# Kernel tuning notes

Measured on AMD Instinct MI355X. Metric: run time of the kernel, lower is better.

Reference implementation:

```python
import jax, jax.numpy as jnp
import numpy as np

B, T, F, H, FUT = 64, 512, 64, 512, 96  # batch, past len, features, hidden, future len


def setup_inputs() -> dict:
    key = jax.random.key(0)
    ks = jax.random.split(key, 19)
    s = 1.0 / np.sqrt(H)  # PyTorch LSTM/Linear init scale
    u = lambda k, shape: jax.random.uniform(k, shape, jnp.float32, -s, s)
    inp = {"input_seq": jax.random.normal(ks[0], (B, T, F), jnp.float32)}
    i = 1
    for pre in ("enc", "dec"):
        for l in range(2):
            ins = F if l == 0 else H
            inp[f"{pre}_Wih{l}"] = u(ks[i], (4 * H, ins)); i += 1
            inp[f"{pre}_Whh{l}"] = u(ks[i], (4 * H, H)); i += 1
            inp[f"{pre}_bih{l}"] = u(ks[i], (4 * H,)); i += 1
            inp[f"{pre}_bhh{l}"] = u(ks[i], (4 * H,)); i += 1
    inp["fc_W"] = u(ks[17], (F, H))
    inp["fc_b"] = u(ks[18], (F,))
    return inp


def _cell(x, h, c, Wih, Whh, bih, bhh):
    # PyTorch gate order: i, f, g, o
    g = x @ Wih.T + h @ Whh.T + bih + bhh
    i_, f_, g_, o_ = jnp.split(g, 4, axis=-1)
    c = jax.nn.sigmoid(f_) * c + jax.nn.sigmoid(i_) * jnp.tanh(g_)
    h = jax.nn.sigmoid(o_) * jnp.tanh(c)
    return h, c


def reference(input_seq, enc_Wih0, enc_Whh0, enc_bih0, enc_bhh0,
              enc_Wih1, enc_Whh1, enc_bih1, enc_bhh1,
              dec_Wih0, dec_Whh0, dec_bih0, dec_bhh0,
              dec_Wih1, dec_Whh1, dec_bih1, dec_bhh1,
              fc_W, fc_b):
    b = input_seq.shape[0]
    z = jnp.zeros((b, H), input_seq.dtype)

    def run_layer(x, Wih, Whh, bih, bhh):
        def step(carry, xt):
            h, c = _cell(xt, carry[0], carry[1], Wih, Whh, bih, bhh)
            return (h, c), h
        (h, c), ys = jax.lax.scan(step, (z, z), jnp.swapaxes(x, 0, 1))
        return jnp.swapaxes(ys, 0, 1), h, c

    # encoder (2 layers, eval mode -> no dropout)
    y0, h0, c0 = run_layer(input_seq, enc_Wih0, enc_Whh0, enc_bih0, enc_bhh0)
    _, h1, c1 = run_layer(y0, enc_Wih1, enc_Whh1, enc_bih1, enc_bhh1)

    def dec_step(carry, _):
        x, dh0, dc0, dh1, dc1 = carry
        dh0, dc0 = _cell(x, dh0, dc0, dec_Wih0, dec_Whh0, dec_bih0, dec_bhh0)
        dh1, dc1 = _cell(dh0, dh1, dc1, dec_Wih1, dec_Whh1, dec_bih1, dec_bhh1)
        out = dh1 @ fc_W.T + fc_b
        return (out, dh0, dc0, dh1, dc1), out

    dec_in = input_seq[:, -1, :]
    _, outs = jax.lax.scan(dec_step, (dec_in, h0, c0, h1, c1), None, length=FUT)
    return jnp.swapaxes(outs, 0, 1)  # [B, FUT, F]
```

## Files before the change

### kernel.cpp

```cpp
#include <hip/hip_runtime.h>
#include <stdint.h>

typedef __attribute__((ext_vector_type(8))) short short8;
typedef __attribute__((ext_vector_type(4))) float floatx4;
typedef unsigned short u16;
typedef unsigned int u32;

constexpr int BSZ = 64;
constexpr int SEQT = 512;
constexpr int FIN = 64;
constexpr int HID = 512;
constexpr int NG = 2048;
constexpr int FUTL = 96;
constexpr int K0 = FIN + HID;
constexpr int K1 = HID + HID;
constexpr int K0P = K0 + 8;
constexpr int NGRP = 256;
constexpr int NFCB = 4;
constexpr int NBLK = NGRP + NFCB;
constexpr int NTHR = 256;

constexpr int SLOT_HP = 128 * 256;
constexpr int SLOT_XP = 16 * 256;
constexpr int NSLOT_H = 65;

constexpr size_t S_W0 = (size_t)NG * K0 * 2;
constexpr size_t S_W1 = (size_t)NG * K1 * 2;
constexpr size_t S_FC = (size_t)FIN * HID * 2;

constexpr size_t OFF_WHI_E0 = 0;
constexpr size_t OFF_WLO_E0 = OFF_WHI_E0 + S_W0;
constexpr size_t OFF_WHI_E1 = OFF_WLO_E0 + S_W0;
constexpr size_t OFF_WLO_E1 = OFF_WHI_E1 + S_W1;
constexpr size_t OFF_WHI_D1 = OFF_WLO_E1 + S_W1;
constexpr size_t OFF_WLO_D1 = OFF_WHI_D1 + S_W1;
constexpr size_t OFF_WFH   = OFF_WLO_D1 + S_W1;
constexpr size_t OFF_WFL   = OFF_WFH + S_W1;
constexpr size_t OFF_FCHI  = OFF_WFL + S_W1;
constexpr size_t OFF_FCLO  = OFF_FCHI + S_FC;
constexpr size_t OFF_GX    = OFF_FCLO + S_FC;
constexpr size_t OFF_BEFF  = OFF_GX + (size_t)NG * BSZ * 4;
constexpr size_t OFF_XP    = OFF_BEFF + (size_t)NG * 4;
constexpr size_t OFF_H0P   = OFF_XP + (size_t)SEQT * SLOT_XP * 4;
constexpr size_t OFF_H1P   = OFF_H0P + (size_t)NSLOT_H * SLOT_HP * 4;
constexpr size_t OFF_CNT   = OFF_H1P + (size_t)NSLOT_H * SLOT_HP * 4;
constexpr size_t CNT_BYTES = 65536;

#define FCF(c)   ((c) + 0)
#define DONE0(c) ((c) + 256)
#define DONE1(c) ((c) + 2304)
#define GOA0(c)  ((c) + 4352)
#define GOB0(c)  ((c) + 6400)
#define GOA1(c)  ((c) + 8448)
#define GOB1(c)  ((c) + 10496)

__device__ __forceinline__ u16 f2bf(float f) {
  u32 u = __float_as_uint(f);
  u += 0x7FFFu + ((u >> 16) & 1u);
  return (u16)(u >> 16);
}
__device__ __forceinline__ float bf2f(u16 h) { return __uint_as_float(((u32)h) << 16); }
__device__ __forceinline__ u32 packsplit(float v) {
  u16 h = f2bf(v);
  u16 l = f2bf(v - bf2f(h));
  return (u32)h | ((u32)l << 16);
}

__device__ __forceinline__ float sigf(float x) { return 1.f / (1.f + __expf(-x)); }
__device__ __forceinline__ float tanh_f(float x) {
  float xx = fminf(20.f, fmaxf(-20.f, x));
  float e = __expf(-2.f * xx);
  return (1.f - e) / (1.f + e);
}

__device__ __forceinline__ floatx4 mfma3(short8 ah, short8 al, short8 bh, short8 bl, floatx4 acc) {
  acc = __builtin_amdgcn_mfma_f32_16x16x32_bf16(ah, bh, acc, 0, 0, 0);
  acc = __builtin_amdgcn_mfma_f32_16x16x32_bf16(ah, bl, acc, 0, 0, 0);
  acc = __builtin_amdgcn_mfma_f32_16x16x32_bf16(al, bh, acc, 0, 0, 0);
  return acc;
}

__device__ __forceinline__ void st_sc_u32(u32* p, u32 v) {
  asm volatile("global_store_dword %0, %1, off sc0 sc1" :: "v"(p), "v"(v) : "memory");
}
#define WAITVM0() asm volatile("s_waitcnt vmcnt(0)" ::: "memory")

#define ALD(p) __hip_atomic_load((p), __ATOMIC_RELAXED, __HIP_MEMORY_SCOPE_AGENT)
#define AST(p, v) __hip_atomic_store((p), (v), __ATOMIC_RELAXED, __HIP_MEMORY_SCOPE_AGENT)

__device__ __forceinline__ int slotof(int u) { return u < 0 ? 0 : ((u & 63) + 1); }

__device__ __forceinline__ void ld_frag(const u32* p, short8& ah, short8& al) {
  uint4 a = *(const uint4*)p;
  uint4 b = *(const uint4*)(p + 256);
  union { u32 u[4]; short8 s; } H, L;
  H.u[0] = __builtin_amdgcn_perm(a.y, a.x, 0x05040100u);
  L.u[0] = __builtin_amdgcn_perm(a.y, a.x, 0x07060302u);
  H.u[1] = __builtin_amdgcn_perm(a.w, a.z, 0x05040100u);
  L.u[1] = __builtin_amdgcn_perm(a.w, a.z, 0x07060302u);
  H.u[2] = __builtin_amdgcn_perm(b.y, b.x, 0x05040100u);
  L.u[2] = __builtin_amdgcn_perm(b.y, b.x, 0x07060302u);
  H.u[3] = __builtin_amdgcn_perm(b.w, b.z, 0x05040100u);
  L.u[3] = __builtin_amdgcn_perm(b.w, b.z, 0x07060302u);
  ah = H.s; al = L.s;
}

__global__ void k_split_pair(const float* __restrict__ Wih, const float* __restrict__ Whh,
                             int ins, int K, u16* __restrict__ hi, u16* __restrict__ lo) {
  int n = NG * K;
  for (int idx = blockIdx.x * blockDim.x + threadIdx.x; idx < n; idx += gridDim.x * blockDim.x) {
    int row = idx / K;
    int k = idx - row * K;
    float v = (k < ins) ? Wih[row * ins + k] : Whh[row * HID + (k - ins)];
    u16 h = f2bf(v);
    hi[idx] = h;
    lo[idx] = f2bf(v - bf2f(h));
  }
}

__global__ void k_split_flat(const float* __restrict__ src, u16* __restrict__ hi,
                             u16* __restrict__ lo, int n) {
  for (int idx = blockIdx.x * blockDim.x + threadIdx.x; idx < n; idx += gridDim.x * blockDim.x) {
    float v = src[idx];
    u16 h = f2bf(v);
    hi[idx] = h;
    lo[idx] = f2bf(v - bf2f(h));
  }
}

__global__ void k_fuse(const float* __restrict__ dWih0, const float* __restrict__ dWhh0,
                       const float* __restrict__ fcW,
                       u16* __restrict__ wfh, u16* __restrict__ wfl) {
  __shared__ float wr[FIN];
  const int row = blockIdx.x;
  if (threadIdx.x < FIN) wr[threadIdx.x] = dWih0[row * FIN + threadIdx.x];
  __syncthreads();
  for (int j = threadIdx.x; j < HID; j += blockDim.x) {
    float acc = 0.f;
#pragma unroll
    for (int f = 0; f < FIN; ++f) acc = fmaf(wr[f], fcW[f * HID + j], acc);
    u16 h = f2bf(acc);
    wfh[(size_t)row * K1 + j] = h;
    wfl[(size_t)row * K1 + j] = f2bf(acc - bf2f(h));
    float v2 = dWhh0[row * HID + j];
    u16 h2 = f2bf(v2);
    wfh[(size_t)row * K1 + HID + j] = h2;
    wfl[(size_t)row * K1 + HID + j] = f2bf(v2 - bf2f(h2));
  }
}

__global__ void k_gx(const float* __restrict__ dWih0, const float* __restrict__ in_seq,
                     const float* __restrict__ fcb, const float* __restrict__ bdih0,
                     const float* __restrict__ bdhh0, float* __restrict__ gx,
                     float* __restrict__ beff) {
  __shared__ float xl[BSZ * FIN];
  __shared__ float fb[FIN];
  const int row0 = blockIdx.x * 8;
  for (int i = threadIdx.x; i < BSZ * FIN; i += blockDim.x) {
    int b = i >> 6, f = i & 63;
    xl[i] = in_seq[(b * SEQT + (SEQT - 1)) * FIN + f];
  }
  if (threadIdx.x < FIN) fb[threadIdx.x] = fcb[threadIdx.x];
  __syncthreads();
  for (int i = threadIdx.x; i < 8 * BSZ; i += blockDim.x) {
    int r = row0 + (i >> 6);
    int b = i & 63;
    float acc = 0.f;
#pragma unroll 8
    for (int f = 0; f < FIN; ++f)
      acc = fmaf(dWih0[r * FIN + f], xl[(b << 6) + f] - fb[f], acc);
    gx[r * BSZ + b] = acc;
    if (b == 0) {
      float accb = 0.f;
#pragma unroll 8
      for (int f = 0; f < FIN; ++f) accb = fmaf(dWih0[r * FIN + f], fb[f], accb);
      beff[r] = bdih0[r] + bdhh0[r] + accb;
    }
  }
}

__global__ void k_pack_x(const float* __restrict__ x, u32* __restrict__ xp) {
  int n = BSZ * SEQT * FIN;
  for (int idx = blockIdx.x * blockDim.x + threadIdx.x; idx < n; idx += gridDim.x * blockDim.x) {
    int t = idx / (BSZ * FIN);
    int rem = idx - t * (BSZ * FIN);
    int b = rem >> 6;
    int f = rem & 63;
    u32 pk = packsplit(x[(b * SEQT + t) * FIN + f]);
    int off = ((f >> 2) * 64 + b) * 4 + (f & 3);
    xp[t * SLOT_XP + off] = pk;
  }
}

struct Params {
  const u16 *we0h, *we0l, *we1h, *we1l;
  const u16 *wd1h, *wd1l, *wfh, *wfl;
  const u16 *fch, *fcl;
  const u32 *xp;
  u32 *h0p, *h1p;
  const float *beih0, *behh0, *beih1, *behh1;
  const float *bdih1, *bdhh1;
  const float *gx, *beff;
  const float *fcb;
  float *out;
  u32 *cnt;
};

__device__ void master_wait(u32* own, u32 ownT, u32* fcf, u32 fcT) {
  if (threadIdx.x < 64) {
    int l = threadIdx.x;
    for (;;) {
      bool ok = ALD(own + l * 16) >= ownT && ALD(own + (l + 64) * 16) >= ownT;
      if (fcf && l < 4) ok = ok && ALD(fcf + l * 16) >= fcT;
      if (__all(ok)) break;
      __builtin_amdgcn_s_sleep(1);
    }
  }
  __syncthreads();
}

__device__ void sweep128(u32* arr, u32 T) {
  if (threadIdx.x < 64) {
    int l = threadIdx.x;
    while (!__all(ALD(arr + l * 16) >= T && ALD(arr + (l + 64) * 16) >= T))
      __builtin_amdgcn_s_sleep(1);
  }
  __syncthreads();
}

__device__ __forceinline__ void worker_wait(u32* cell, u32 tok) {
  if (threadIdx.x == 0) {
    while (ALD(cell) < tok) __builtin_amdgcn_s_sleep(1);
  }
  __syncthreads();
}

__device__ __forceinline__ void fence_acq() {
  __builtin_amdgcn_fence(__ATOMIC_ACQUIRE, "agent");
}

__device__ __forceinline__ void arrive(u32* cell, u32 tok) {
  WAITVM0();
  __syncthreads();
  if (threadIdx.x == 0) AST(cell, tok);
}

__device__ __forceinline__ void bcast(u32* goA, u32 tokA, u32* goBF, u32 prog) {
  const int tid = threadIdx.x;
  if (tid >= 1 && tid < 128) AST(goA + (tid << 4), tokA);
  else if (tid >= 128) AST(goBF + ((tid - 128) << 4), prog);
}

template <bool IS_L1>
__device__ void load_w_lds(const u16* __restrict__ gh, const u16* __restrict__ gl,
                           u16* wh, u16* wl, int hc) {
  constexpr int K = IS_L1 ? K1 : K0;
  for (int i = threadIdx.x; i < 16 * K; i += NTHR) {
    int rr, k;
    if (IS_L1) { rr = i >> 10; k = i & 1023; }
    else       { rr = i / K0;  k = i - rr * K0; }
    int gc = ((rr >> 2) * HID) + hc + (rr & 3);
    int dst = IS_L1 ? ((rr << 10) + ((((k >> 3) ^ rr)) << 3) + (k & 7))
                    : (rr * K0P + k);
    wh[dst] = gh[(size_t)gc * K + k];
    wl[dst] = gl[(size_t)gc * K + k];
  }
  __syncthreads();
}

template <bool IS_L1, int KBASE, int LEN>
__device__ __forceinline__ void kpart(const u32* __restrict__ sp,
                                      const u16* __restrict__ wh, const u16* __restrict__ wl,
                                      int r, int quad, int mo, floatx4& acc) {
  const int qo = quad << 3;
  constexpr int NIT = LEN / 32;
  uint4 ra[NIT], rb[NIT];
#pragma unroll
  for (int i = 0; i < NIT; ++i) {
    const u32* p = sp + (((i * 32 + qo) >> 2) << 8) + mo;
    ra[i] = *(const uint4*)p;
    rb[i] = *(const uint4*)(p + 256);
  }
#pragma unroll
  for (int i = 0; i < NIT; ++i) {
    union { u32 u[4]; short8 s; } H, L;
    H.u[0] = __builtin_amdgcn_perm(ra[i].y, ra[i].x, 0x05040100u);
    L.u[0] = __builtin_amdgcn_perm(ra[i].y, ra[i].x, 0x07060302u);
    H.u[1] = __builtin_amdgcn_perm(ra[i].w, ra[i].z, 0x05040100u);
    L.u[1] = __builtin_amdgcn_perm(ra[i].w, ra[i].z, 0x07060302u);
    H.u[2] = __builtin_amdgcn_perm(rb[i].y, rb[i].x, 0x05040100u);
    L.u[2] = __builtin_amdgcn_perm(rb[i].y, rb[i].x, 0x07060302u);
    H.u[3] = __builtin_amdgcn_perm(rb[i].w, rb[i].z, 0x05040100u);
    L.u[3] = __builtin_amdgcn_perm(rb[i].w, rb[i].z, 0x07060302u);
    const int kg = i * 32 + KBASE;
    int woff;
    if (IS_L1) { int c = (kg >> 3) + quad; woff = (r << 10) + ((c ^ r) << 3); }
    else       { woff = r * K0P + kg + qo; }
    short8 bh = *(const short8*)(wh + woff);
    short8 bl = *(const short8*)(wl + woff);
    acc = mfma3(H.s, L.s, bh, bl, acc);
  }
}

__device__ __forceinline__ void epilogue(floatx4 acc, floatx4 bs, float& creg,
                                         u32* __restrict__ oslab,
                                         const float* __restrict__ gxb) {
  const int tid = threadIdx.x, lane = tid & 63;
  const int j = lane & 3;
  const int isel = (lane >> 2) & 3;
  const int slb = lane & 48;
  float gate[4];
#pragma unroll
  for (int q = 0; q < 4; ++q) {
    const int sl = slb + (q << 2) + j;
    float t0 = __shfl(acc[0], sl, 64);
    float t1 = __shfl(acc[1], sl, 64);
    float t2 = __shfl(acc[2], sl, 64);
    float t3 = __shfl(acc[3], sl, 64);
    gate[q] = (isel == 0) ? t0 : (isel == 1) ? t1 : (isel == 2) ? t2 : t3;
  }
  if (gxb != nullptr) {
    const int bb = tid >> 2;
#pragma unroll
    for (int q = 0; q < 4; ++q) gate[q] += gxb[q * (HID * BSZ) + j * BSZ + bb];
  }
  float iv = gate[0] + bs[0];
  float fv = gate[1] + bs[1];
  float gv = gate[2] + bs[2];
  float ov = gate[3] + bs[3];
  float cn = fmaf(sigf(fv), creg, sigf(iv) * tanh_f(gv));
  float hn = sigf(ov) * tanh_f(cn);
  creg = cn;
  st_sc_u32(oslab + tid, packsplit(hn));
}

__device__ void fc_step(int t, int blkq, const u32* __restrict__ h1slot,
                        const u16* __restrict__ fh, const u16* __restrict__ fl,
                        const float* __restrict__ fcb, float* __restrict__ out) {
  const int tid = threadIdx.x, lane = tid & 63, w = tid >> 6;
  const int quad = lane >> 4, r = lane & 15;
  const int m = (w << 4) + r;
  const int qo = quad << 3;
  const int mo = m << 2;
  const int col = (blkq << 4) + r;
  floatx4 acc = {0.f, 0.f, 0.f, 0.f};
#pragma unroll
  for (int kk = 0; kk < HID; kk += 32) {
    short8 ah, al;
    ld_frag(h1slot + (((kk + qo) >> 2) << 8) + mo, ah, al);
    short8 b1 = *(const short8*)(fh + col * HID + kk + qo);
    short8 b2 = *(const short8*)(fl + col * HID + kk + qo);
    acc = mfma3(ah, al, b1, b2, acc);
  }
  float bias = fcb[col];
#pragma unroll
  for (int i = 0; i < 4; ++i) {
    int b = (w << 4) + (quad << 2) + i;
    out[(b * FUTL + t) * FIN + col] = acc[i] + bias;
  }
}

__global__ __launch_bounds__(NTHR, 1) void lstm_coop(Params p) {
  __shared__ u16 wsmem[32768];
  u16* wh = wsmem;
  u16* wl = wsmem + 16 * 1024;
  const int blk = blockIdx.x;
  const int tid = threadIdx.x;

  u32* fcf = FCF(p.cnt);
  u32* d0 = DONE0(p.cnt);
  u32* d1 = DONE1(p.cnt);

  if (blk >= NGRP) {
    const int fi = blk - NGRP;
    for (int t = 0; t < FUTL; ++t) {
      sweep128(d1, (u32)(513 + t));
      if ((t & 63) == 0) fence_acq();
      fc_step(t, fi, p.h1p + (size_t)slotof(512 + t) * SLOT_HP,
              p.fch, p.fcl, p.fcb, p.out);
      WAITVM0();
      __syncthreads();
      if (tid == 0) AST(fcf + fi * 16, (u32)(t + 1));
    }
    return;
  }

  const int grp = blk >> 7;
  const int lidx = blk & 127;
  const int hc = lidx << 2;
  const int lane = tid & 63, w = tid >> 6;
  const int quad = lane >> 4, r = lane & 15;
  const int mo = ((w << 4) + r) << 2;

  u32* goA  = grp ? GOA1(p.cnt) : GOA0(p.cnt);
  u32* goBF = grp ? GOB0(p.cnt) : GOB1(p.cnt);
  u32* myGoA = goA + lidx * 16;
  u32* myGoB = (grp ? GOB1(p.cnt) : GOB0(p.cnt)) + lidx * 16;
  u32* myDone = (grp ? d1 : d0) + lidx * 16;

  floatx4 bse, bsd;
  {
    int ch = hc + (tid & 3);
    const float* bi  = grp ? p.beih1 : p.beih0;
    const float* bh2 = grp ? p.behh1 : p.behh0;
#pragma unroll
    for (int q = 0; q < 4; ++q) {
      bse[q] = bi[q * HID + ch] + bh2[q * HID + ch];
      bsd[q] = grp ? (p.bdih1[q * HID + ch] + p.bdhh1[q * HID + ch])
                   : p.beff[q * HID + ch];
    }
  }
  float creg = 0.f;

  if (!grp) {
    load_w_lds<false>(p.we0h, p.we0l, wh, wl, hc);
    for (int s = 0; s < SEQT; ++s) {
      u32 tok = (u32)(s + 1);
      floatx4 acc = {0.f, 0.f, 0.f, 0.f};
      if (lidx == 0) {
        master_wait(d0, (u32)s, nullptr, 0u);
        if (s >= 63) worker_wait(myGoB, (u32)(s - 63));
        bcast(goA, tok, goBF, (u32)s);
        if ((s & 63) == 0 && s) fence_acq();
        kpart<false, 0, FIN>(p.xp + (size_t)s * SLOT_XP, wh, wl, r, quad, mo, acc);
      } else {
        kpart<false, 0, FIN>(p.xp + (size_t)s * SLOT_XP, wh, wl, r, quad, mo, acc);
        worker_wait(myGoA, tok);
        if ((s & 63) == 0 && s) fence_acq();
      }
      kpart<false, FIN, HID>(p.h0p + (size_t)slotof(s - 1) * SLOT_HP, wh, wl, r, quad, mo, acc);
      epilogue(acc, bse, creg,
               p.h0p + (size_t)slotof(s) * SLOT_HP + (lidx << 8), nullptr);
      arrive(myDone, tok);
    }
    if (lidx == 0) {
      sweep128(d0, 512u);
      if (tid >= 128) AST(goBF + ((tid - 128) << 4), 512u);
    }
    load_w_lds<true>(p.wfh, p.wfl, wh, wl, hc);
    for (int t = 0; t < FUTL; ++t) {
      u32 tok = (u32)(513 + t);
      floatx4 acc = {0.f, 0.f, 0.f, 0.f};
      if (lidx == 0) {
        master_wait(d0, (u32)(512 + t), nullptr, 0u);
        if (t == 0) worker_wait(myGoB, 449u);
        bcast(goA, tok, goBF, (u32)(512 + t));
      } else {
        worker_wait(myGoA, tok);
      }
      if ((t & 63) == 0) fence_acq();
      kpart<true, 512, HID>(p.h0p + (size_t)slotof(511 + t) * SLOT_HP, wh, wl, r, quad, mo, acc);
      if (t) {
        worker_wait(myGoB, (u32)(512 + t));
        kpart<true, 0, HID>(p.h1p + (size_t)slotof(511 + t) * SLOT_HP, wh, wl, r, quad, mo, acc);
      }
      epilogue(acc, bsd, creg,
               p.h0p + (size_t)slotof(512 + t) * SLOT_HP + (lidx << 8),
               (t == 0) ? (p.gx + hc * BSZ) : nullptr);
      arrive(myDone, tok);
    }
    if (lidx == 0) {
      sweep128(d0, 608u);
      if (tid >= 128) AST(goBF + ((tid - 128) << 4), 608u);
    }
  } else {
    load_w_lds<true>(p.we1h, p.we1l, wh, wl, hc);
    for (int t = 0; t < SEQT; ++t) {
      u32 tok = (u32)(t + 1);
      floatx4 acc = {0.f, 0.f, 0.f, 0.f};
      if (lidx == 0) {
        master_wait(d1, (u32)t, nullptr, 0u);
        bcast(goA, tok, goBF, (u32)t);
      } else {
        worker_wait(myGoA, tok);
      }
      if ((t & 63) == 0 && t) fence_acq();
      kpart<true, 512, HID>(p.h1p + (size_t)slotof(t - 1) * SLOT_HP, wh, wl, r, quad, mo, acc);
      worker_wait(myGoB, (u32)(t + 1));
      kpart<true, 0, HID>(p.h0p + (size_t)slotof(t) * SLOT_HP, wh, wl, r, quad, mo, acc);
      epilogue(acc, bse, creg,
               p.h1p + (size_t)slotof(t) * SLOT_HP + (lidx << 8), nullptr);
      arrive(myDone, tok);
    }
    load_w_lds<true>(p.wd1h, p.wd1l, wh, wl, hc);
    for (int t = 0; t < FUTL; ++t) {
      u32 tok = (u32)(513 + t);
      floatx4 acc = {0.f, 0.f, 0.f, 0.f};
      if (lidx == 0) {
        master_wait(d1, (u32)(512 + t), (t >= 64) ? fcf : nullptr, (u32)(t - 63));
        bcast(goA, tok, goBF, (u32)(512 + t));
      } else {
        worker_wait(myGoA, tok);
      }
      if ((t & 63) == 0) fence_acq();
      kpart<true, 512, HID>(p.h1p + (size_t)slotof(511 + t) * SLOT_HP, wh, wl, r, quad, mo, acc);
      worker_wait(myGoB, (u32)(513 + t));
      kpart<true, 0, HID>(p.h0p + (size_t)slotof(512 + t) * SLOT_HP, wh, wl, r, quad, mo, acc);
      epilogue(acc, bsd, creg,
               p.h1p + (size_t)slotof(512 + t) * SLOT_HP + (lidx << 8), nullptr);
      arrive(myDone, tok);
    }
  }
}

extern "C" void kernel_launch(void* const* d_in, const int* in_sizes, int n_in,
                              void* d_out, int out_size, void* d_ws, size_t ws_size,
                              hipStream_t stream) {
  (void)in_sizes; (void)n_in; (void)out_size; (void)ws_size;
  const float* in_seq = (const float*)d_in[0];
  const float* eWih0 = (const float*)d_in[1];
  const float* eWhh0 = (const float*)d_in[2];
  const float* ebih0 = (const float*)d_in[3];
  const float* ebhh0 = (const float*)d_in[4];
  const float* eWih1 = (const float*)d_in[5];
  const float* eWhh1 = (const float*)d_in[6];
  const float* ebih1 = (const float*)d_in[7];
  const float* ebhh1 = (const float*)d_in[8];
  const float* dWih0 = (const float*)d_in[9];
  const float* dWhh0 = (const float*)d_in[10];
  const float* dbih0 = (const float*)d_in[11];
  const float* dbhh0 = (const float*)d_in[12];
  const float* dWih1 = (const float*)d_in[13];
  const float* dWhh1 = (const float*)d_in[14];
  const float* dbih1 = (const float*)d_in[15];
  const float* dbhh1 = (const float*)d_in[16];
  const float* fcW  = (const float*)d_in[17];
  const float* fcb  = (const float*)d_in[18];

  char* ws = (char*)d_ws;
  u16* we0h = (u16*)(ws + OFF_WHI_E0); u16* we0l = (u16*)(ws + OFF_WLO_E0);
  u16* we1h = (u16*)(ws + OFF_WHI_E1); u16* we1l = (u16*)(ws + OFF_WLO_E1);
  u16* wd1h = (u16*)(ws + OFF_WHI_D1); u16* wd1l = (u16*)(ws + OFF_WLO_D1);
  u16* wfh  = (u16*)(ws + OFF_WFH);    u16* wfl  = (u16*)(ws + OFF_WFL);
  u16* fch  = (u16*)(ws + OFF_FCHI);   u16* fcl  = (u16*)(ws + OFF_FCLO);
  float* gx   = (float*)(ws + OFF_GX);
  float* beff = (float*)(ws + OFF_BEFF);
  u32* xp   = (u32*)(ws + OFF_XP);
  u32* h0p  = (u32*)(ws + OFF_H0P);
  u32* h1p  = (u32*)(ws + OFF_H1P);
  u32* cnt  = (u32*)(ws + OFF_CNT);

  hipMemsetAsync(ws + OFF_H0P, 0, (size_t)SLOT_HP * 4, stream);
  hipMemsetAsync(ws + OFF_H1P, 0, (size_t)SLOT_HP * 4, stream);
  hipMemsetAsync(ws + OFF_CNT, 0, CNT_BYTES, stream);

  k_split_pair<<<512, 256, 0, stream>>>(eWih0, eWhh0, FIN, K0, we0h, we0l);
  k_split_pair<<<512, 256, 0, stream>>>(eWih1, eWhh1, HID, K1, we1h, we1l);
  k_split_pair<<<512, 256, 0, stream>>>(dWih1, dWhh1, HID, K1, wd1h, wd1l);
  k_split_flat<<<128, 256, 0, stream>>>(fcW, fch, fcl, FIN * HID);
  k_fuse<<<NG, 256, 0, stream>>>(dWih0, dWhh0, fcW, wfh, wfl);
  k_gx<<<256, 256, 0, stream>>>(dWih0, in_seq, fcb, dbih0, dbhh0, gx, beff);
  k_pack_x<<<1024, 256, 0, stream>>>(in_seq, xp);

  Params p;
  p.we0h = we0h; p.we0l = we0l; p.we1h = we1h; p.we1l = we1l;
  p.wd1h = wd1h; p.wd1l = wd1l; p.wfh = wfh; p.wfl = wfl;
  p.fch = fch; p.fcl = fcl;
  p.xp = xp; p.h0p = h0p; p.h1p = h1p;
  p.beih0 = ebih0; p.behh0 = ebhh0; p.beih1 = ebih1; p.behh1 = ebhh1;
  p.bdih1 = dbih1; p.bdhh1 = dbhh1;
  p.gx = gx; p.beff = beff;
  p.fcb = fcb;
  p.out = (float*)d_out;
  p.cnt = cnt;

  lstm_coop<<<dim3(NBLK), dim3(NTHR), 0, stream>>>(p);
}
```

Measured before the change: 4.272 ms.

## Reorder layer-1 encoder waits, cache progress tokens, drop spin sleeps

Removes s_sleep from the spin-wait loops so waiters react to flag changes sooner. Adds cached-token variants of the waits so a block skips re-polling a counter it has already seen past the target. In the layer-1 encoder loop, non-master blocks now do the input (h0) half of the matvec before waiting on their own layer's go signal, overlapping that work with the layer-1 barrier. The fc-progress check is split out of master_wait into a single-thread wait. Busy spinning without sleep may add memory traffic and contention on the flag cache lines.

```diff
diff --git a/kernel.cpp b/kernel.cpp
--- a/kernel.cpp
+++ b/kernel.cpp
@@ -206,15 +206,10 @@
   u32 *cnt;
 };
 
-__device__ void master_wait(u32* own, u32 ownT, u32* fcf, u32 fcT) {
+__device__ void master_wait(u32* own, u32 ownT) {
   if (threadIdx.x < 64) {
     int l = threadIdx.x;
-    for (;;) {
-      bool ok = ALD(own + l * 16) >= ownT && ALD(own + (l + 64) * 16) >= ownT;
-      if (fcf && l < 4) ok = ok && ALD(fcf + l * 16) >= fcT;
-      if (__all(ok)) break;
-      __builtin_amdgcn_s_sleep(1);
-    }
+    while (!__all(ALD(own + l * 16) >= ownT && ALD(own + (l + 64) * 16) >= ownT)) {}
   }
   __syncthreads();
 }
@@ -230,7 +225,29 @@
 
 __device__ __forceinline__ void worker_wait(u32* cell, u32 tok) {
   if (threadIdx.x == 0) {
-    while (ALD(cell) < tok) __builtin_amdgcn_s_sleep(1);
+    while (ALD(cell) < tok) {}
+  }
+  __syncthreads();
+}
+
+__device__ __forceinline__ void worker_wait_c(u32* cell, u32 tok, u32& cache) {
+  if (threadIdx.x == 0 && cache < tok) {
+    u32 v;
+    do { v = ALD(cell); } while (v < tok);
+    cache = v;
+  }
+  __syncthreads();
+}
+
+__device__ __forceinline__ void fcf_wait_c(u32* fcf, u32 tok, u32& cache) {
+  if (threadIdx.x == 0 && cache < tok) {
+    u32 m;
+    do {
+      u32 a = ALD(fcf), b = ALD(fcf + 16), c = ALD(fcf + 32), d = ALD(fcf + 48);
+      u32 m1 = a < b ? a : b, m2 = c < d ? c : d;
+      m = m1 < m2 ? m1 : m2;
+    } while (m < tok);
+    cache = m;
   }
   __syncthreads();
 }
@@ -413,13 +430,14 @@
   float creg = 0.f;
 
   if (!grp) {
+    u32 d1seen = 0;
     load_w_lds<false>(p.we0h, p.we0l, wh, wl, hc);
     for (int s = 0; s < SEQT; ++s) {
       u32 tok = (u32)(s + 1);
       floatx4 acc = {0.f, 0.f, 0.f, 0.f};
       if (lidx == 0) {
-        master_wait(d0, (u32)s, nullptr, 0u);
-        if (s >= 63) worker_wait(myGoB, (u32)(s - 63));
+        master_wait(d0, (u32)s);
+        if (s >= 63) worker_wait_c(myGoB, (u32)(s - 63), d1seen);
         bcast(goA, tok, goBF, (u32)s);
         if ((s & 63) == 0 && s) fence_acq();
         kpart<false, 0, FIN>(p.xp + (size_t)s * SLOT_XP, wh, wl, r, quad, mo, acc);
@@ -442,8 +460,8 @@
       u32 tok = (u32)(513 + t);
       floatx4 acc = {0.f, 0.f, 0.f, 0.f};
       if (lidx == 0) {
-        master_wait(d0, (u32)(512 + t), nullptr, 0u);
-        if (t == 0) worker_wait(myGoB, 449u);
+        master_wait(d0, (u32)(512 + t));
+        if (t == 0) worker_wait_c(myGoB, 449u, d1seen);
         bcast(goA, tok, goBF, (u32)(512 + t));
       } else {
         worker_wait(myGoA, tok);
@@ -451,7 +469,7 @@
       if ((t & 63) == 0) fence_acq();
       kpart<true, 512, HID>(p.h0p + (size_t)slotof(511 + t) * SLOT_HP, wh, wl, r, quad, mo, acc);
       if (t) {
-        worker_wait(myGoB, (u32)(512 + t));
+        worker_wait_c(myGoB, (u32)(512 + t), d1seen);
         kpart<true, 0, HID>(p.h1p + (size_t)slotof(511 + t) * SLOT_HP, wh, wl, r, quad, mo, acc);
       }
       epilogue(acc, bsd, creg,
@@ -464,20 +482,26 @@
       if (tid >= 128) AST(goBF + ((tid - 128) << 4), 608u);
     }
   } else {
+    u32 d0seen = 0;
+    u32 fcseen = 0;
     load_w_lds<true>(p.we1h, p.we1l, wh, wl, hc);
     for (int t = 0; t < SEQT; ++t) {
       u32 tok = (u32)(t + 1);
       floatx4 acc = {0.f, 0.f, 0.f, 0.f};
       if (lidx == 0) {
-        master_wait(d1, (u32)t, nullptr, 0u);
+        master_wait(d1, (u32)t);
         bcast(goA, tok, goBF, (u32)t);
+        worker_wait_c(myGoB, (u32)(t + 1), d0seen);
+        if ((t & 63) == 0 && t) fence_acq();
+        kpart<true, 0, HID>(p.h0p + (size_t)slotof(t) * SLOT_HP, wh, wl, r, quad, mo, acc);
+        kpart<true, 512, HID>(p.h1p + (size_t)slotof(t - 1) * SLOT_HP, wh, wl, r, quad, mo, acc);
       } else {
+        worker_wait_c(myGoB, (u32)(t + 1), d0seen);
+        if ((t & 63) == 0 && t) fence_acq();
+        kpart<true, 0, HID>(p.h0p + (size_t)slotof(t) * SLOT_HP, wh, wl, r, quad, mo, acc);
         worker_wait(myGoA, tok);
+        kpart<true, 512, HID>(p.h1p + (size_t)slotof(t - 1) * SLOT_HP, wh, wl, r, quad, mo, acc);
       }
-      if ((t & 63) == 0 && t) fence_acq();
-      kpart<true, 512, HID>(p.h1p + (size_t)slotof(t - 1) * SLOT_HP, wh, wl, r, quad, mo, acc);
-      worker_wait(myGoB, (u32)(t + 1));
-      kpart<true, 0, HID>(p.h0p + (size_t)slotof(t) * SLOT_HP, wh, wl, r, quad, mo, acc);
       epilogue(acc, bse, creg,
                p.h1p + (size_t)slotof(t) * SLOT_HP + (lidx << 8), nullptr);
       arrive(myDone, tok);
@@ -487,14 +511,15 @@
       u32 tok = (u32)(513 + t);
       floatx4 acc = {0.f, 0.f, 0.f, 0.f};
       if (lidx == 0) {
-        master_wait(d1, (u32)(512 + t), (t >= 64) ? fcf : nullptr, (u32)(t - 63));
+        master_wait(d1, (u32)(512 + t));
+        if (t >= 64) fcf_wait_c(fcf, (u32)(t - 63), fcseen);
         bcast(goA, tok, goBF, (u32)(512 + t));
       } else {
         worker_wait(myGoA, tok);
       }
       if ((t & 63) == 0) fence_acq();
       kpart<true, 512, HID>(p.h1p + (size_t)slotof(511 + t) * SLOT_HP, wh, wl, r, quad, mo, acc);
-      worker_wait(myGoB, (u32)(513 + t));
+      worker_wait_c(myGoB, (u32)(513 + t), d0seen);
       kpart<true, 0, HID>(p.h0p + (size_t)slotof(512 + t) * SLOT_HP, wh, wl, r, quad, mo, acc);
       epilogue(acc, bsd, creg,
                p.h1p + (size_t)slotof(512 + t) * SLOT_HP + (lidx << 8), nullptr);
```

Result: faster. 3.529 ms (median of 2 runs) (-17.4%).

## Restructure inter-block synchronization with packed progress counters and dedicated masters

Applied to the files above, without the earlier changes.

Replaces the per-block padded done flags and the two-level go-flag broadcast with packed progress arrays (one u32 per block, contiguous). Dedicated master loops run on spare FC blocks for the encoder phases. Other waits sweep the packed arrays directly, cache the observed minimum so repeated sweeps can be skipped, and drop the s_sleep backoff. The layer-1 encoder also reorders its two partial matmuls so the h0 input term is computed before waiting on its own recurrence. The aim is to cut per-step barrier latency on the serial recurrence. The cost is more polling traffic on adjacent words, and the change risks contention or ordering bugs in the reworked protocol.

```diff
diff --git a/kernel.cpp b/kernel.cpp
--- a/kernel.cpp
+++ b/kernel.cpp
@@ -47,12 +47,10 @@
 constexpr size_t CNT_BYTES = 65536;
 
 #define FCF(c)   ((c) + 0)
-#define DONE0(c) ((c) + 256)
-#define DONE1(c) ((c) + 2304)
-#define GOA0(c)  ((c) + 4352)
-#define GOB0(c)  ((c) + 6400)
-#define GOA1(c)  ((c) + 8448)
-#define GOB1(c)  ((c) + 10496)
+#define PK0(c)   ((c) + 256)
+#define PK1(c)   ((c) + 384)
+#define GOA0(c)  ((c) + 512)
+#define GOA1(c)  ((c) + 2560)
 
 __device__ __forceinline__ u16 f2bf(float f) {
   u32 u = __float_as_uint(f);
@@ -206,23 +204,27 @@
   u32 *cnt;
 };
 
-__device__ void master_wait(u32* own, u32 ownT, u32* fcf, u32 fcT) {
+__device__ __forceinline__ void sweep_pk_c(const u32* pk, u32 target, u32& cache) {
+  if (threadIdx.x < 64 && cache < target) {
+    u32 a, b;
+    do {
+      a = ALD(pk + threadIdx.x);
+      b = ALD(pk + threadIdx.x + 64);
+    } while (!__all(a >= target && b >= target));
+    u32 m = a < b ? a : b;
+#pragma unroll
+    for (int off = 1; off < 64; off <<= 1) {
+      u32 o = __shfl_xor(m, off, 64);
+      m = o < m ? o : m;
+    }
+    cache = m;
+  }
+  __syncthreads();
+}
+
+__device__ void sweep_pk_sleep(const u32* pk, u32 target) {
   if (threadIdx.x < 64) {
-    int l = threadIdx.x;
-    for (;;) {
-      bool ok = ALD(own + l * 16) >= ownT && ALD(own + (l + 64) * 16) >= ownT;
-      if (fcf && l < 4) ok = ok && ALD(fcf + l * 16) >= fcT;
-      if (__all(ok)) break;
-      __builtin_amdgcn_s_sleep(1);
-    }
-  }
-  __syncthreads();
-}
-
-__device__ void sweep128(u32* arr, u32 T) {
-  if (threadIdx.x < 64) {
-    int l = threadIdx.x;
-    while (!__all(ALD(arr + l * 16) >= T && ALD(arr + (l + 64) * 16) >= T))
+    while (!__all(ALD(pk + threadIdx.x) >= target && ALD(pk + threadIdx.x + 64) >= target))
       __builtin_amdgcn_s_sleep(1);
   }
   __syncthreads();
@@ -230,7 +232,20 @@
 
 __device__ __forceinline__ void worker_wait(u32* cell, u32 tok) {
   if (threadIdx.x == 0) {
-    while (ALD(cell) < tok) __builtin_amdgcn_s_sleep(1);
+    while (ALD(cell) < tok) {}
+  }
+  __syncthreads();
+}
+
+__device__ __forceinline__ void fcf_wait_c(u32* fcf, u32 tok, u32& cache) {
+  if (threadIdx.x == 0 && cache < tok) {
+    u32 m;
+    do {
+      u32 a = ALD(fcf), b = ALD(fcf + 16), c = ALD(fcf + 32), d = ALD(fcf + 48);
+      u32 m1 = a < b ? a : b, m2 = c < d ? c : d;
+      m = m1 < m2 ? m1 : m2;
+    } while (m < tok);
+    cache = m;
   }
   __syncthreads();
 }
@@ -245,10 +260,23 @@
   if (threadIdx.x == 0) AST(cell, tok);
 }
 
-__device__ __forceinline__ void bcast(u32* goA, u32 tokA, u32* goBF, u32 prog) {
-  const int tid = threadIdx.x;
-  if (tid >= 1 && tid < 128) AST(goA + (tid << 4), tokA);
-  else if (tid >= 128) AST(goBF + ((tid - 128) << 4), prog);
+__device__ void enc_master(const u32* pkOwn, const u32* pkFore, u32* goA, bool farlag) {
+  for (int s = 0; s < SEQT; ++s) {
+    if (threadIdx.x < 64) {
+      int l = threadIdx.x;
+      for (;;) {
+        bool ok = ALD(pkOwn + l) >= (u32)s && ALD(pkOwn + l + 64) >= (u32)s;
+        if (farlag && s >= 63) {
+          u32 ft = (u32)(s - 63);
+          ok = ok && ALD(pkFore + l) >= ft && ALD(pkFore + l + 64) >= ft;
+        }
+        if (__all(ok)) break;
+      }
+    }
+    __syncthreads();
+    if (threadIdx.x < 128) AST(goA + (threadIdx.x << 4), (u32)(s + 1));
+    __syncthreads();
+  }
 }
 
 template <bool IS_L1>
@@ -368,13 +396,15 @@
   const int tid = threadIdx.x;
 
   u32* fcf = FCF(p.cnt);
-  u32* d0 = DONE0(p.cnt);
-  u32* d1 = DONE1(p.cnt);
+  u32* pk0 = PK0(p.cnt);
+  u32* pk1 = PK1(p.cnt);
 
   if (blk >= NGRP) {
     const int fi = blk - NGRP;
+    if (fi == 0) enc_master(pk0, pk1, GOA0(p.cnt), true);
+    if (fi == 1) enc_master(pk1, pk0, GOA1(p.cnt), false);
     for (int t = 0; t < FUTL; ++t) {
-      sweep128(d1, (u32)(513 + t));
+      sweep_pk_sleep(pk1, (u32)(513 + t));
       if ((t & 63) == 0) fence_acq();
       fc_step(t, fi, p.h1p + (size_t)slotof(512 + t) * SLOT_HP,
               p.fch, p.fcl, p.fcb, p.out);
@@ -392,11 +422,8 @@
   const int quad = lane >> 4, r = lane & 15;
   const int mo = ((w << 4) + r) << 2;
 
-  u32* goA  = grp ? GOA1(p.cnt) : GOA0(p.cnt);
-  u32* goBF = grp ? GOB0(p.cnt) : GOB1(p.cnt);
-  u32* myGoA = goA + lidx * 16;
-  u32* myGoB = (grp ? GOB1(p.cnt) : GOB0(p.cnt)) + lidx * 16;
-  u32* myDone = (grp ? d1 : d0) + lidx * 16;
+  u32* myGoA = (grp ? GOA1(p.cnt) : GOA0(p.cnt)) + lidx * 16;
+  u32* myPk  = (grp ? pk1 : pk0) + lidx;
 
   floatx4 bse, bsd;
   {
@@ -413,92 +440,61 @@
   float creg = 0.f;
 
   if (!grp) {
+    u32 cpk0 = 0, cpk1 = 0;
     load_w_lds<false>(p.we0h, p.we0l, wh, wl, hc);
     for (int s = 0; s < SEQT; ++s) {
-      u32 tok = (u32)(s + 1);
       floatx4 acc = {0.f, 0.f, 0.f, 0.f};
-      if (lidx == 0) {
-        master_wait(d0, (u32)s, nullptr, 0u);
-        if (s >= 63) worker_wait(myGoB, (u32)(s - 63));
-        bcast(goA, tok, goBF, (u32)s);
-        if ((s & 63) == 0 && s) fence_acq();
-        kpart<false, 0, FIN>(p.xp + (size_t)s * SLOT_XP, wh, wl, r, quad, mo, acc);
-      } else {
-        kpart<false, 0, FIN>(p.xp + (size_t)s * SLOT_XP, wh, wl, r, quad, mo, acc);
-        worker_wait(myGoA, tok);
-        if ((s & 63) == 0 && s) fence_acq();
-      }
+      kpart<false, 0, FIN>(p.xp + (size_t)s * SLOT_XP, wh, wl, r, quad, mo, acc);
+      worker_wait(myGoA, (u32)(s + 1));
+      if ((s & 63) == 0 && s) fence_acq();
       kpart<false, FIN, HID>(p.h0p + (size_t)slotof(s - 1) * SLOT_HP, wh, wl, r, quad, mo, acc);
       epilogue(acc, bse, creg,
                p.h0p + (size_t)slotof(s) * SLOT_HP + (lidx << 8), nullptr);
-      arrive(myDone, tok);
-    }
-    if (lidx == 0) {
-      sweep128(d0, 512u);
-      if (tid >= 128) AST(goBF + ((tid - 128) << 4), 512u);
+      arrive(myPk, (u32)(s + 1));
     }
     load_w_lds<true>(p.wfh, p.wfl, wh, wl, hc);
     for (int t = 0; t < FUTL; ++t) {
-      u32 tok = (u32)(513 + t);
       floatx4 acc = {0.f, 0.f, 0.f, 0.f};
-      if (lidx == 0) {
-        master_wait(d0, (u32)(512 + t), nullptr, 0u);
-        if (t == 0) worker_wait(myGoB, 449u);
-        bcast(goA, tok, goBF, (u32)(512 + t));
-      } else {
-        worker_wait(myGoA, tok);
-      }
+      sweep_pk_c(pk0, (u32)(512 + t), cpk0);
+      if (t == 0) sweep_pk_c(pk1, 449u, cpk1);
       if ((t & 63) == 0) fence_acq();
       kpart<true, 512, HID>(p.h0p + (size_t)slotof(511 + t) * SLOT_HP, wh, wl, r, quad, mo, acc);
       if (t) {
-        worker_wait(myGoB, (u32)(512 + t));
+        sweep_pk_c(pk1, (u32)(512 + t), cpk1);
         kpart<true, 0, HID>(p.h1p + (size_t)slotof(511 + t) * SLOT_HP, wh, wl, r, quad, mo, acc);
       }
       epilogue(acc, bsd, creg,
                p.h0p + (size_t)slotof(512 + t) * SLOT_HP + (lidx << 8),
                (t == 0) ? (p.gx + hc * BSZ) : nullptr);
-      arrive(myDone, tok);
-    }
-    if (lidx == 0) {
-      sweep128(d0, 608u);
-      if (tid >= 128) AST(goBF + ((tid - 128) << 4), 608u);
+      arrive(myPk, (u32)(513 + t));
     }
   } else {
+    u32 cpk0 = 0, cfc = 0;
     load_w_lds<true>(p.we1h, p.we1l, wh, wl, hc);
     for (int t = 0; t < SEQT; ++t) {
-      u32 tok = (u32)(t + 1);
       floatx4 acc = {0.f, 0.f, 0.f, 0.f};
-      if (lidx == 0) {
-        master_wait(d1, (u32)t, nullptr, 0u);
-        bcast(goA, tok, goBF, (u32)t);
-      } else {
-        worker_wait(myGoA, tok);
-      }
+      sweep_pk_c(pk0, (u32)(t + 1), cpk0);
       if ((t & 63) == 0 && t) fence_acq();
+      kpart<true, 0, HID>(p.h0p + (size_t)slotof(t) * SLOT_HP, wh, wl, r, quad, mo, acc);
+      worker_wait(myGoA, (u32)(t + 1));
       kpart<true, 512, HID>(p.h1p + (size_t)slotof(t - 1) * SLOT_HP, wh, wl, r, quad, mo, acc);
-      worker_wait(myGoB, (u32)(t + 1));
-      kpart<true, 0, HID>(p.h0p + (size_t)slotof(t) * SLOT_HP, wh, wl, r, quad, mo, acc);
       epilogue(acc, bse, creg,
                p.h1p + (size_t)slotof(t) * SLOT_HP + (lidx << 8), nullptr);
-      arrive(myDone, tok);
-    }
+      arrive(myPk, (u32)(t + 1));
+    }
+    u32 cpk1own = 0;
     load_w_lds<true>(p.wd1h, p.wd1l, wh, wl, hc);
     for (int t = 0; t < FUTL; ++t) {
-      u32 tok = (u32)(513 + t);
       floatx4 acc = {0.f, 0.f, 0.f, 0.f};
-      if (lidx == 0) {
-        master_wait(d1, (u32)(512 + t), (t >= 64) ? fcf : nullptr, (u32)(t - 63));
-        bcast(goA, tok, goBF, (u32)(512 + t));
-      } else {
-        worker_wait(myGoA, tok);
-      }
+      sweep_pk_c(pk1, (u32)(512 + t), cpk1own);
+      if (t >= 64 && (t & 15) == 0) fcf_wait_c(fcf, (u32)(t - 48), cfc);
       if ((t & 63) == 0) fence_acq();
       kpart<true, 512, HID>(p.h1p + (size_t)slotof(511 + t) * SLOT_HP, wh, wl, r, quad, mo, acc);
-      worker_wait(myGoB, (u32)(513 + t));
+      sweep_pk_c(pk0, (u32)(513 + t), cpk0);
       kpart<true, 0, HID>(p.h0p + (size_t)slotof(512 + t) * SLOT_HP, wh, wl, r, quad, mo, acc);
       epilogue(acc, bsd, creg,
                p.h1p + (size_t)slotof(512 + t) * SLOT_HP + (lidx << 8), nullptr);
-      arrive(myDone, tok);
+      arrive(myPk, (u32)(513 + t));
     }
   }
 }
```

Result: faster. 4.019 ms (-5.9%).
